# Optimization experiments

Hardware: AMD Instinct MI355X
Metric: run time of the kernel (lower is better)

Reference implementation:

```python
import jax, jax.numpy as jnp
import numpy as np

N, E, D, K, NCONV = 50000, 800000, 64, 3, 6


def setup_inputs() -> dict:
    key = jax.random.key(0)
    ks = jax.random.split(key, 6)
    X = jax.random.normal(ks[0], (N, D), jnp.float32)
    edge_index = jax.random.randint(ks[1], (2, E), 0, N, dtype=jnp.int64)
    edge_weight = jax.random.uniform(ks[2], (E,), jnp.float32)
    H = jax.random.normal(ks[3], (N, D), jnp.float32)
    lambda_max = jnp.ones((1,), jnp.float32) * 2.0  # typical sym-normalized Laplacian bound
    conv_w = jax.random.normal(ks[4], (NCONV, K, D, D), jnp.float32) / np.sqrt(D)
    conv_b = jnp.zeros((NCONV, D), jnp.float32)
    return {"X": X, "edge_index": edge_index, "edge_weight": edge_weight,
            "H": H, "lambda_max": lambda_max, "conv_w": conv_w, "conv_b": conv_b}


def reference(X, edge_index, edge_weight, H, lambda_max, conv_w, conv_b):
    src, dst = edge_index[0], edge_index[1]
    # symmetric normalization: norm_e = w_e / sqrt(deg_src * deg_dst)
    deg = jax.ops.segment_sum(edge_weight, src, num_segments=N)
    dinv = jnp.where(deg > 0, deg ** -0.5, 0.0)
    norm = edge_weight * dinv[src] * dinv[dst]  # [E]
    lam = lambda_max.reshape(())
    c = 2.0 / lam

    def a_prop(v):  # A_norm @ v via scatter-add over edges, [N,D]
        return jax.ops.segment_sum(norm[:, None] * v[src], dst, num_segments=N)

    def l_hat(v):  # (2/lam)(I - A_norm) v - v
        return (c - 1.0) * v - c * a_prop(v)

    def cheb(v, w, b):  # ChebConv order K: sum_k T_k(L_hat) v @ W_k + b
        tx0, tx1 = v, l_hat(v)
        out = tx0 @ w[0] + tx1 @ w[1]
        for k in range(2, K):
            tx2 = 2.0 * l_hat(tx1) - tx0
            out = out + tx2 @ w[k]
            tx0, tx1 = tx1, tx2
        return out + b

    Z = jax.nn.sigmoid(cheb(X, conv_w[0], conv_b[0]) + cheb(H, conv_w[1], conv_b[1]))
    R = jax.nn.sigmoid(cheb(X, conv_w[2], conv_b[2]) + cheb(H, conv_w[3], conv_b[3]))
    H_tilde = jnp.tanh(cheb(X, conv_w[4], conv_b[4]) + cheb(H * R, conv_w[5], conv_b[5]))
    return Z * H_tilde + (1.0 - Z) * H
```

## Files before the change

### kernel.cpp

```cpp
#include <hip/hip_runtime.h>
#include <cstdint>
#include <cstddef>

typedef unsigned int u32;
typedef unsigned short u16;
typedef unsigned long long u64;

#define D 64
#define NCH 512
#define CAP 5120

typedef __attribute__((ext_vector_type(8))) short bf16x8;
typedef __attribute__((ext_vector_type(4))) float f32x4;

static __device__ __forceinline__ float sigmoidf_(float x) {
    return 1.f / (1.f + __expf(-x));
}
static __device__ __forceinline__ u16 f2bf(float x) {
    u32 u = __float_as_uint(x);
    return (u16)((u + 0x7fffu + ((u >> 16) & 1u)) >> 16);
}
static __device__ __forceinline__ u32 packbf2(float a, float b) {
    return (u32)f2bf(a) | ((u32)f2bf(b) << 16);
}
static __device__ __forceinline__ float bflo(u32 u) { return __uint_as_float(u << 16); }
static __device__ __forceinline__ float bfhi(u32 u) { return __uint_as_float(u & 0xffff0000u); }


__global__ void init_kernel(u32* cur_d, u32* cur_s) {
    int t = threadIdx.x;
    cur_d[t] = (u32)(t * CAP);
    cur_s[t] = (u32)(t * CAP);
}

__global__ __launch_bounds__(256) void coarse_kernel(
    const int* __restrict__ src, const int* __restrict__ dst, const float* __restrict__ w,
    u32* cur_d, u32* cur_s,
    u64* __restrict__ slab_d, u32* __restrict__ slab_s,
    int E, int CE) {
    __shared__ u32 hd[256], hs[256], cd[256], cs[256];
    int t = threadIdx.x, c = blockIdx.x;
    hd[t] = 0; hs[t] = 0;
    __syncthreads();
    int e0 = c * CE, e1 = min(E, e0 + CE);
    for (int e = e0 + t; e < e1; e += 256) {
        atomicAdd(&hd[(u32)dst[e] >> 8], 1u);
        atomicAdd(&hs[(u32)src[e] >> 8], 1u);
    }
    __syncthreads();
    cd[t] = atomicAdd(&cur_d[t], hd[t]);
    cs[t] = atomicAdd(&cur_s[t], hs[t]);
    __syncthreads();
    for (int e = e0 + t; e < e1; e += 256) {
        int s = src[e], d = dst[e];
        u32 wb = (u32)f2bf(w[e]);
        u32 pd = atomicAdd(&cd[(u32)d >> 8], 1u);
        u32 ps = atomicAdd(&cs[(u32)s >> 8], 1u);
        if (pd < (u32)(((d >> 8) + 1) * CAP))
            slab_d[pd] = (u64)((u32)s | (((u32)d & 255u) << 16)) | ((u64)wb << 32);
        if (ps < (u32)(((s >> 8) + 1) * CAP))
            slab_s[ps] = ((u32)s & 255u) | (wb << 16);
    }
}

__global__ void bprefix_kernel(const u32* __restrict__ cur_d, u32* __restrict__ bstart, int NB) {
    __shared__ int sd[256];
    int t = threadIdx.x;
    int v = (t < NB) ? min((int)cur_d[t] - t * CAP, CAP) : 0;
    sd[t] = v;
    __syncthreads();
    for (int o = 1; o < 256; o <<= 1) {
        int a = (t >= o) ? sd[t - o] : 0;
        __syncthreads();
        sd[t] += a;
        __syncthreads();
    }
    bstart[t] = (u32)(sd[t] - v);
}

__global__ __launch_bounds__(256) void fine_dst_kernel(
    const u64* __restrict__ slab, const u32* __restrict__ cur_d,
    const u32* __restrict__ bstart, u32* __restrict__ edge4,
    int* __restrict__ cnt, int* __restrict__ row_start, int N_) {
    __shared__ int h[256], sd[256], cur[256];
    int b = blockIdx.x, t = threadIdx.x;
    int m = min((int)cur_d[b] - b * CAP, CAP);
    const u64* rp = slab + (size_t)b * CAP;
    h[t] = 0;
    __syncthreads();
    for (int i = t; i < m; i += 256) atomicAdd(&h[(int)((rp[i] >> 16) & 255u)], 1);
    __syncthreads();
    int v = h[t];
    sd[t] = v;
    __syncthreads();
    for (int o = 1; o < 256; o <<= 1) {
        int a = (t >= o) ? sd[t - o] : 0;
        __syncthreads();
        sd[t] += a;
        __syncthreads();
    }
    int excl = sd[t] - v;
    cur[t] = excl;
    int bs = (int)bstart[b];
    int node = (b << 8) + t;
    if (node < N_) { cnt[node] = v; row_start[node] = bs + excl; }
    __syncthreads();
    for (int i = t; i < m; i += 256) {
        u64 r = rp[i];
        int f = (int)((r >> 16) & 255u);
        int p = atomicAdd(&cur[f], 1);
        edge4[bs + p] = (u32)(r & 0xffffu) | ((u32)(r >> 32) << 16);
    }
}

__global__ __launch_bounds__(256) void fine_deg_kernel(
    const u32* __restrict__ slab_s, const u32* __restrict__ cur_s,
    float* __restrict__ dinv, int N_) {
    __shared__ float dg[256];
    int b = blockIdx.x, t = threadIdx.x;
    int m = min((int)cur_s[b] - b * CAP, CAP);
    const u32* rp = slab_s + (size_t)b * CAP;
    dg[t] = 0.f;
    __syncthreads();
    for (int i = t; i < m; i += 256) {
        u32 r = rp[i];
        atomicAdd(&dg[r & 255u], __uint_as_float(r & 0xffff0000u));
    }
    __syncthreads();
    int node = (b << 8) + t;
    if (node < N_) dinv[node] = (dg[t] > 0.f) ? rsqrtf(dg[t]) : 0.f;
}


__global__ void xh2_kernel(const float* __restrict__ X, const float* __restrict__ H,
                           const float* __restrict__ dinv,
                           u32* __restrict__ XH_u, u32* __restrict__ XH_t, int total) {
    int i = blockIdx.x * blockDim.x + threadIdx.x;
    if (i >= total) return;
    int nn = i >> 6, l = i & 63;
    const float* sp = (l < 32 ? X : H) + (size_t)nn * 64 + ((2 * l) & 63);
    float2 v = *(const float2*)sp;
    float dv = dinv[nn];
    XH_t[i] = packbf2(v.x, v.y);
    XH_u[i] = packbf2(v.x * dv, v.y * dv);
}

__global__ __launch_bounds__(256) void wt_kernel(const float* __restrict__ w, u32* __restrict__ WT) {
    __shared__ float s[64][68];
    int g = blockIdx.x, t = threadIdx.x;
    const float* wp = w + (size_t)g * 4096;
    for (int i = t; i < 1024; i += 256) {
        int k = i >> 4, c4 = (i & 15) * 4;
        *(float4*)&s[k][c4] = *(const float4*)&wp[k * 64 + c4];
    }
    __syncthreads();
    for (int i = t; i < 2048; i += 256) {
        int uk = i & 31, n = i >> 5;
        WT[(size_t)g * 2048 + n * 32 + uk] = packbf2(s[2 * uk][n], s[2 * uk + 1][n]);
    }
}


__global__ __launch_bounds__(256) void lhat128_kernel(
    const u32* __restrict__ vu, const u32* __restrict__ vt, const u32* __restrict__ w0t,
    u32* __restrict__ out_t, u32* __restrict__ out_u,
    const int* __restrict__ rs, const int* __restrict__ cnt, const float* __restrict__ dinv,
    const u32* __restrict__ edges, const float* __restrict__ lam_ptr, int n) {
    int node = (blockIdx.x * blockDim.x + threadIdx.x) >> 6;
    if (node >= n) return;
    int l = threadIdx.x & 63;
    int g = l >> 4, f = l & 15;
    int e0 = rs[node], end = e0 + cnt[node];
    float acc[8];
#pragma unroll
    for (int j = 0; j < 8; j++) acc[j] = 0.f;

    int base = e0;
    for (; base + 16 <= end; base += 16) {
        u32 r0 = edges[base + g];
        u32 r1 = edges[base + 4 + g];
        u32 r2 = edges[base + 8 + g];
        u32 r3 = edges[base + 12 + g];
        const uint4 q0 = *(const uint4*)(vu + (size_t)(r0 & 0xffffu) * 64 + 4 * f);
        const uint4 q1 = *(const uint4*)(vu + (size_t)(r1 & 0xffffu) * 64 + 4 * f);
        const uint4 q2 = *(const uint4*)(vu + (size_t)(r2 & 0xffffu) * 64 + 4 * f);
        const uint4 q3 = *(const uint4*)(vu + (size_t)(r3 & 0xffffu) * 64 + 4 * f);
        float n0 = __uint_as_float(r0 & 0xffff0000u);
        float n1 = __uint_as_float(r1 & 0xffff0000u);
        float n2 = __uint_as_float(r2 & 0xffff0000u);
        float n3 = __uint_as_float(r3 & 0xffff0000u);
        acc[0] += n0 * bflo(q0.x); acc[1] += n0 * bfhi(q0.x);
        acc[2] += n0 * bflo(q0.y); acc[3] += n0 * bfhi(q0.y);
        acc[4] += n0 * bflo(q0.z); acc[5] += n0 * bfhi(q0.z);
        acc[6] += n0 * bflo(q0.w); acc[7] += n0 * bfhi(q0.w);
        acc[0] += n1 * bflo(q1.x); acc[1] += n1 * bfhi(q1.x);
        acc[2] += n1 * bflo(q1.y); acc[3] += n1 * bfhi(q1.y);
        acc[4] += n1 * bflo(q1.z); acc[5] += n1 * bfhi(q1.z);
        acc[6] += n1 * bflo(q1.w); acc[7] += n1 * bfhi(q1.w);
        acc[0] += n2 * bflo(q2.x); acc[1] += n2 * bfhi(q2.x);
        acc[2] += n2 * bflo(q2.y); acc[3] += n2 * bfhi(q2.y);
        acc[4] += n2 * bflo(q2.z); acc[5] += n2 * bfhi(q2.z);
        acc[6] += n2 * bflo(q2.w); acc[7] += n2 * bfhi(q2.w);
        acc[0] += n3 * bflo(q3.x); acc[1] += n3 * bfhi(q3.x);
        acc[2] += n3 * bflo(q3.y); acc[3] += n3 * bfhi(q3.y);
        acc[4] += n3 * bflo(q3.z); acc[5] += n3 * bfhi(q3.z);
        acc[6] += n3 * bflo(q3.w); acc[7] += n3 * bfhi(q3.w);
    }
    for (; base < end; base += 4) {
        int ei = base + g;
        u32 r0 = (ei < end) ? edges[ei] : 0u;
        const uint4 q0 = *(const uint4*)(vu + (size_t)(r0 & 0xffffu) * 64 + 4 * f);
        float n0 = __uint_as_float(r0 & 0xffff0000u);
        acc[0] += n0 * bflo(q0.x); acc[1] += n0 * bfhi(q0.x);
        acc[2] += n0 * bflo(q0.y); acc[3] += n0 * bfhi(q0.y);
        acc[4] += n0 * bflo(q0.z); acc[5] += n0 * bfhi(q0.z);
        acc[6] += n0 * bflo(q0.w); acc[7] += n0 * bfhi(q0.w);
    }
#pragma unroll
    for (int m = 16; m <= 32; m <<= 1)
#pragma unroll
        for (int j = 0; j < 8; j++) acc[j] += __shfl_xor(acc[j], m);

    const uint4 sv = *(const uint4*)(vt + (size_t)node * 64 + 4 * f);
    float self[8];
    self[0] = bflo(sv.x); self[1] = bfhi(sv.x);
    self[2] = bflo(sv.y); self[3] = bfhi(sv.y);
    self[4] = bflo(sv.z); self[5] = bfhi(sv.z);
    self[6] = bflo(sv.w); self[7] = bfhi(sv.w);
    float c = 2.f / lam_ptr[0];
    float dv = dinv[node];
    float rx[8];
#pragma unroll
    for (int j = 0; j < 8; j++) rx[j] = (c - 1.f) * self[j] - (c * dv) * acc[j];
    if (w0t) {
        const uint4 wv4 = *(const uint4*)(w0t + (size_t)node * 64 + 4 * f);
        rx[0] = 2.f * rx[0] - bflo(wv4.x); rx[1] = 2.f * rx[1] - bfhi(wv4.x);
        rx[2] = 2.f * rx[2] - bflo(wv4.y); rx[3] = 2.f * rx[3] - bfhi(wv4.y);
        rx[4] = 2.f * rx[4] - bflo(wv4.z); rx[5] = 2.f * rx[5] - bfhi(wv4.z);
        rx[6] = 2.f * rx[6] - bflo(wv4.w); rx[7] = 2.f * rx[7] - bfhi(wv4.w);
    }
    if (l < 16) {
        uint4 o;
        o.x = packbf2(rx[0], rx[1]); o.y = packbf2(rx[2], rx[3]);
        o.z = packbf2(rx[4], rx[5]); o.w = packbf2(rx[6], rx[7]);
        *(uint4*)(out_t + (size_t)node * 64 + 4 * f) = o;
        if (out_u) {
            uint4 ou;
            ou.x = packbf2(rx[0] * dv, rx[1] * dv); ou.y = packbf2(rx[2] * dv, rx[3] * dv);
            ou.z = packbf2(rx[4] * dv, rx[5] * dv); ou.w = packbf2(rx[6] * dv, rx[7] * dv);
            *(uint4*)(out_u + (size_t)node * 64 + 4 * f) = ou;
        }
    }
}

__global__ __launch_bounds__(256) void lhat64_kernel(
    const u32* __restrict__ vu, const u32* __restrict__ vt, const u32* __restrict__ w0t,
    u32* __restrict__ out_t, u32* __restrict__ out_u,
    const int* __restrict__ rs, const int* __restrict__ cnt, const float* __restrict__ dinv,
    const u32* __restrict__ edges, const float* __restrict__ lam_ptr, int n) {
    int node = (blockIdx.x * blockDim.x + threadIdx.x) >> 6;
    if (node >= n) return;
    int l = threadIdx.x & 63;
    int g = l >> 3, f = l & 7;
    int e0 = rs[node], end = e0 + cnt[node];
    float acc[8];
#pragma unroll
    for (int j = 0; j < 8; j++) acc[j] = 0.f;

    int base = e0;
    for (; base + 16 <= end; base += 16) {
        u32 r0 = edges[base + g];
        u32 r1 = edges[base + 8 + g];
        const uint4 q0 = *(const uint4*)(vu + (size_t)(r0 & 0xffffu) * 32 + 4 * f);
        const uint4 q1 = *(const uint4*)(vu + (size_t)(r1 & 0xffffu) * 32 + 4 * f);
        float n0 = __uint_as_float(r0 & 0xffff0000u);
        float n1 = __uint_as_float(r1 & 0xffff0000u);
        acc[0] += n0 * bflo(q0.x); acc[1] += n0 * bfhi(q0.x);
        acc[2] += n0 * bflo(q0.y); acc[3] += n0 * bfhi(q0.y);
        acc[4] += n0 * bflo(q0.z); acc[5] += n0 * bfhi(q0.z);
        acc[6] += n0 * bflo(q0.w); acc[7] += n0 * bfhi(q0.w);
        acc[0] += n1 * bflo(q1.x); acc[1] += n1 * bfhi(q1.x);
        acc[2] += n1 * bflo(q1.y); acc[3] += n1 * bfhi(q1.y);
        acc[4] += n1 * bflo(q1.z); acc[5] += n1 * bfhi(q1.z);
        acc[6] += n1 * bflo(q1.w); acc[7] += n1 * bfhi(q1.w);
    }
    for (; base < end; base += 8) {
        int ei = base + g;
        u32 r0 = (ei < end) ? edges[ei] : 0u;
        const uint4 q0 = *(const uint4*)(vu + (size_t)(r0 & 0xffffu) * 32 + 4 * f);
        float n0 = __uint_as_float(r0 & 0xffff0000u);
        acc[0] += n0 * bflo(q0.x); acc[1] += n0 * bfhi(q0.x);
        acc[2] += n0 * bflo(q0.y); acc[3] += n0 * bfhi(q0.y);
        acc[4] += n0 * bflo(q0.z); acc[5] += n0 * bfhi(q0.z);
        acc[6] += n0 * bflo(q0.w); acc[7] += n0 * bfhi(q0.w);
    }
#pragma unroll
    for (int m = 8; m <= 32; m <<= 1)
#pragma unroll
        for (int j = 0; j < 8; j++) acc[j] += __shfl_xor(acc[j], m);

    const uint4 sv = *(const uint4*)(vt + (size_t)node * 32 + 4 * f);
    float self[8];
    self[0] = bflo(sv.x); self[1] = bfhi(sv.x);
    self[2] = bflo(sv.y); self[3] = bfhi(sv.y);
    self[4] = bflo(sv.z); self[5] = bfhi(sv.z);
    self[6] = bflo(sv.w); self[7] = bfhi(sv.w);
    float c = 2.f / lam_ptr[0];
    float dv = dinv[node];
    float rx[8];
#pragma unroll
    for (int j = 0; j < 8; j++) rx[j] = (c - 1.f) * self[j] - (c * dv) * acc[j];
    if (w0t) {
        const uint4 wv4 = *(const uint4*)(w0t + (size_t)node * 32 + 4 * f);
        rx[0] = 2.f * rx[0] - bflo(wv4.x); rx[1] = 2.f * rx[1] - bfhi(wv4.x);
        rx[2] = 2.f * rx[2] - bflo(wv4.y); rx[3] = 2.f * rx[3] - bfhi(wv4.y);
        rx[4] = 2.f * rx[4] - bflo(wv4.z); rx[5] = 2.f * rx[5] - bfhi(wv4.z);
        rx[6] = 2.f * rx[6] - bflo(wv4.w); rx[7] = 2.f * rx[7] - bfhi(wv4.w);
    }
    if (l < 8) {
        uint4 o;
        o.x = packbf2(rx[0], rx[1]); o.y = packbf2(rx[2], rx[3]);
        o.z = packbf2(rx[4], rx[5]); o.w = packbf2(rx[6], rx[7]);
        *(uint4*)(out_t + (size_t)node * 32 + 4 * f) = o;
        if (out_u) {
            uint4 ou;
            ou.x = packbf2(rx[0] * dv, rx[1] * dv); ou.y = packbf2(rx[2] * dv, rx[3] * dv);
            ou.z = packbf2(rx[4] * dv, rx[5] * dv); ou.w = packbf2(rx[6] * dv, rx[7] * dv);
            *(uint4*)(out_u + (size_t)node * 32 + 4 * f) = ou;
        }
    }
}

__global__ __launch_bounds__(256) void gemm_mfma_kernel(
    const u32* __restrict__ A0, const u32* __restrict__ A1, const u32* __restrict__ A2,
    int strideU, int colOffU,
    const u32* __restrict__ WT,
    float* __restrict__ out, int out_ld, int cg0, int cg1, int cg2, int n) {
    __shared__ u32 As[128][20];
    __shared__ u32 Ws[64][20];
    int t = threadIdx.x;
    int wv = t >> 6, l = t & 63;
    int q = l >> 4, ml = l & 15;
    int gate = blockIdx.y;
    int cg = (gate == 0) ? cg0 : ((gate == 1) ? cg1 : cg2);
    int r0 = blockIdx.x * 128;

    f32x4 acc[2][4];
#pragma unroll
    for (int mi = 0; mi < 2; mi++)
#pragma unroll
        for (int ni = 0; ni < 4; ni++) acc[mi][ni] = (f32x4){0.f, 0.f, 0.f, 0.f};

    for (int kt = 0; kt < 3; kt++) {
        const u32* Ap = (kt == 0) ? A0 : ((kt == 1) ? A1 : A2);
        const u32* Wp = WT + (size_t)(cg * 3 + kt) * 2048;
        for (int h = 0; h < 2; h++) {
            int ar = t >> 1, ac = (t & 1) * 8;
            int gr = r0 + ar; if (gr >= n) gr = n - 1;
            const u32* gp = Ap + (size_t)gr * strideU + colOffU + h * 16 + ac;
            uint4 a4a = *(const uint4*)gp;
            uint4 a4b = *(const uint4*)(gp + 4);
            int wr = t >> 2, wc = (t & 3) * 4;
            uint4 w4 = *(const uint4*)(Wp + (size_t)wr * 32 + h * 16 + wc);
            __syncthreads();
            *(uint4*)&As[ar][ac] = a4a;
            *(uint4*)&As[ar][ac + 4] = a4b;
            *(uint4*)&Ws[wr][wc] = w4;
            __syncthreads();

            bf16x8 bfr[4];
#pragma unroll
            for (int ni = 0; ni < 4; ni++)
                bfr[ni] = *(const bf16x8*)&Ws[ni * 16 + ml][q * 4];
#pragma unroll
            for (int mi = 0; mi < 2; mi++) {
                bf16x8 af = *(const bf16x8*)&As[wv * 32 + mi * 16 + ml][q * 4];
#pragma unroll
                for (int ni = 0; ni < 4; ni++)
                    acc[mi][ni] = __builtin_amdgcn_mfma_f32_16x16x32_bf16(af, bfr[ni], acc[mi][ni], 0, 0, 0);
            }
        }
    }
#pragma unroll
    for (int mi = 0; mi < 2; mi++)
#pragma unroll
        for (int ni = 0; ni < 4; ni++)
#pragma unroll
            for (int reg = 0; reg < 4; reg++) {
                int row = r0 + wv * 32 + mi * 16 + q * 4 + reg;
                int col = gate * 64 + ni * 16 + ml;
                if (row < n) out[(size_t)row * out_ld + col] = acc[mi][ni][reg];
            }
}


__global__ void gate_kernel(const float* __restrict__ GX, const float* __restrict__ GH,
                            const float* __restrict__ convb, const float* __restrict__ H,
                            const float* __restrict__ dinv,
                            float* __restrict__ Z, u16* __restrict__ HR_t, u16* __restrict__ HR_u,
                            int total) {
    int i = blockIdx.x * blockDim.x + threadIdx.x;
    if (i >= total) return;
    int n = i >> 6, d = i & 63;
    float z = sigmoidf_(GX[(size_t)n * 192 + d] + GH[(size_t)n * 128 + d]
                        + convb[0 * 64 + d] + convb[1 * 64 + d]);
    float r = sigmoidf_(GX[(size_t)n * 192 + 64 + d] + GH[(size_t)n * 128 + 64 + d]
                        + convb[2 * 64 + d] + convb[3 * 64 + d]);
    float hr = H[i] * r;
    float dv = dinv[n];
    Z[i] = z;
    HR_t[i] = f2bf(hr);
    HR_u[i] = f2bf(hr * dv);
}

__global__ __launch_bounds__(256) void gemm_final_kernel(
    const u32* __restrict__ A0, const u32* __restrict__ A1, const u32* __restrict__ A2,
    const u32* __restrict__ WT, const float* __restrict__ convb,
    const float* __restrict__ Zb, const float* __restrict__ GXh, const float* __restrict__ Hf,
    float* __restrict__ outp, int n) {
    __shared__ u32 As[128][36];
    int t = threadIdx.x;
    int wv = t >> 6, l = t & 63;
    int q = l >> 4, ml = l & 15;
    int r0 = blockIdx.x * 128;

    f32x4 S[2][4];
#pragma unroll
    for (int mi = 0; mi < 2; mi++)
#pragma unroll
        for (int ni = 0; ni < 4; ni++) S[mi][ni] = (f32x4){0.f, 0.f, 0.f, 0.f};

    for (int kt = 0; kt < 3; kt++) {
        const u32* Ap = (kt == 0) ? A0 : ((kt == 1) ? A1 : A2);
        int ar = t >> 1, ac = (t & 1) * 16;
        int gr = r0 + ar; if (gr >= n) gr = n - 1;
        const u32* gp = Ap + (size_t)gr * 32 + ac;
        uint4 v0 = *(const uint4*)(gp +  0);
        uint4 v1 = *(const uint4*)(gp +  4);
        uint4 v2 = *(const uint4*)(gp +  8);
        uint4 v3 = *(const uint4*)(gp + 12);
        __syncthreads();
        *(uint4*)&As[ar][ac +  0] = v0;
        *(uint4*)&As[ar][ac +  4] = v1;
        *(uint4*)&As[ar][ac +  8] = v2;
        *(uint4*)&As[ar][ac + 12] = v3;
        __syncthreads();

        const u32* Wp = WT + (size_t)(15 + kt) * 2048 + ml * 32 + q * 4;
#pragma unroll
        for (int h = 0; h < 2; h++) {
            bf16x8 bw[4];
#pragma unroll
            for (int ni = 0; ni < 4; ni++)
                bw[ni] = *(const bf16x8*)(Wp + ni * 512 + h * 16);
#pragma unroll
            for (int mi = 0; mi < 2; mi++) {
                bf16x8 afr = *(const bf16x8*)&As[wv * 32 + mi * 16 + ml][h * 16 + q * 4];
#pragma unroll
                for (int ni = 0; ni < 4; ni++)
                    S[mi][ni] = __builtin_amdgcn_mfma_f32_16x16x32_bf16(afr, bw[ni], S[mi][ni], 0, 0, 0);
            }
        }
    }
#pragma unroll
    for (int ni = 0; ni < 4; ni++) {
        int col = ni * 16 + ml;
        float bh = convb[256 + col] + convb[320 + col];
#pragma unroll
        for (int mi = 0; mi < 2; mi++)
#pragma unroll
            for (int reg = 0; reg < 4; reg++) {
                int row = r0 + wv * 32 + mi * 16 + q * 4 + reg;
                if (row < n) {
                    size_t o = (size_t)row * 64 + col;
                    float z = Zb[o];
                    float ht = tanhf(S[mi][ni][reg] + GXh[(size_t)row * 192 + col] + bh);
                    outp[o] = z * ht + (1.f - z) * Hf[o];
                }
            }
    }
}


extern "C" void kernel_launch(void* const* d_in, const int* in_sizes, int n_in,
                              void* d_out, int out_size, void* d_ws, size_t ws_size,
                              hipStream_t stream) {
    const float* X     = (const float*)d_in[0];
    const int*   ei    = (const int*)d_in[1];
    const float* ew    = (const float*)d_in[2];
    const float* H     = (const float*)d_in[3];
    const float* lam   = (const float*)d_in[4];
    const float* convw = (const float*)d_in[5];
    const float* convb = (const float*)d_in[6];
    float* out = (float*)d_out;

    const int N = in_sizes[0] / D;
    const int E = in_sizes[2];
    const int* src = ei;
    const int* dst = ei + E;

    const int NB = (N + 255) >> 8;
    const int CE = (E + NCH - 1) / NCH;

    char* p = (char*)d_ws;
    auto alloc = [&](size_t bytes) {
        void* r = (void*)p;
        p += (bytes + 255) & ~(size_t)255;
        return r;
    };
    float* GX   = (float*)alloc((size_t)N * 192 * 4);
    float* GH   = (float*)alloc((size_t)N * 128 * 4);
    float* Zb   = (float*)alloc((size_t)N * 64 * 4);
    u32* XH_u = (u32*)alloc((size_t)N * 64 * 4);
    u32* XH_t = (u32*)alloc((size_t)N * 64 * 4);
    u32* T1_u = (u32*)alloc((size_t)N * 64 * 4);
    u32* T1_t = (u32*)alloc((size_t)N * 64 * 4);
    u32* T2_t = (u32*)alloc((size_t)N * 64 * 4);
    u16* HR_u = (u16*)alloc((size_t)N * 64 * 2);
    u16* HR_t = (u16*)alloc((size_t)N * 64 * 2);
    u16* U1_u = (u16*)alloc((size_t)N * 64 * 2);
    u16* U1_t = (u16*)alloc((size_t)N * 64 * 2);
    u16* U2_t = (u16*)alloc((size_t)N * 64 * 2);
    u32* edge4 = (u32*)alloc((size_t)E * 4);
    u64* slab_d = (u64*)alloc((size_t)NB * CAP * 8);
    u32* slab_s = (u32*)alloc((size_t)NB * CAP * 4);
    u32* cur_d  = (u32*)alloc(256 * 4);
    u32* cur_s  = (u32*)alloc(256 * 4);
    u32* bstart = (u32*)alloc(256 * 4);
    int* cnt       = (int*)alloc((size_t)N * 4);
    int* row_start = (int*)alloc((size_t)N * 4);
    float* dinv    = (float*)alloc((size_t)N * 4);
    u32* WT = (u32*)alloc((size_t)18 * 2048 * 4);

    const int BLK = 256;
    const int gND  = (N * D + BLK - 1) / BLK;
    const int gWav = gND;
    const int gx   = (N + 127) / 128;

    init_kernel<<<1, 256, 0, stream>>>(cur_d, cur_s);
    coarse_kernel<<<NCH, BLK, 0, stream>>>(src, dst, ew, cur_d, cur_s, slab_d, slab_s, E, CE);
    bprefix_kernel<<<1, 256, 0, stream>>>(cur_d, bstart, NB);
    fine_dst_kernel<<<NB, BLK, 0, stream>>>(slab_d, cur_d, bstart, edge4, cnt, row_start, N);
    fine_deg_kernel<<<NB, BLK, 0, stream>>>(slab_s, cur_s, dinv, N);

    wt_kernel<<<18, BLK, 0, stream>>>(convw, WT);
    xh2_kernel<<<gND, BLK, 0, stream>>>(X, H, dinv, XH_u, XH_t, N * D);

    lhat128_kernel<<<gWav, BLK, 0, stream>>>(XH_u, XH_t, nullptr, T1_t, T1_u,
                                             row_start, cnt, dinv, edge4, lam, N);
    lhat128_kernel<<<gWav, BLK, 0, stream>>>(T1_u, T1_t, XH_t, T2_t, nullptr,
                                             row_start, cnt, dinv, edge4, lam, N);
    gemm_mfma_kernel<<<dim3(gx, 3), BLK, 0, stream>>>(XH_t, T1_t, T2_t, 64, 0, WT, GX, 192, 0, 2, 4, N);
    gemm_mfma_kernel<<<dim3(gx, 2), BLK, 0, stream>>>(XH_t, T1_t, T2_t, 64, 32, WT, GH, 128, 1, 3, 3, N);

    gate_kernel<<<gND, BLK, 0, stream>>>(GX, GH, convb, H, dinv, Zb, HR_t, HR_u, N * D);

    lhat64_kernel<<<gWav, BLK, 0, stream>>>((const u32*)HR_u, (const u32*)HR_t, nullptr,
                                            (u32*)U1_t, (u32*)U1_u,
                                            row_start, cnt, dinv, edge4, lam, N);
    lhat64_kernel<<<gWav, BLK, 0, stream>>>((const u32*)U1_u, (const u32*)U1_t, (const u32*)HR_t,
                                            (u32*)U2_t, nullptr,
                                            row_start, cnt, dinv, edge4, lam, N);

    gemm_final_kernel<<<gx, BLK, 0, stream>>>((const u32*)HR_t, (const u32*)U1_t, (const u32*)U2_t,
                                              WT, convb, Zb, GX + 128, H, out, N);
}
```

Measured before the change: 347.4 us.

## Fuse both gate GEMMs with sigmoid gate epilogue into one kernel

Replaces the two gemm_mfma launches (X-side and H-side gates) and the separate gate_kernel with a single kernel. Each block loads the full 128-column XH/T1/T2 row once and accumulates all five conv weight groups into three gate accumulators. It then applies the sigmoid gates and writes Z, H*R and the X-side candidate pre-activation directly. This removes the fp32 GX/GH intermediates and their round trips through global memory, at the cost of more accumulator registers per thread and weights read from global or L2 instead of shared memory.

```diff
diff --git a/kernel.cpp b/kernel.cpp
--- a/kernel.cpp
+++ b/kernel.cpp
@@ -331,92 +331,107 @@
     }
 }
 
-__global__ __launch_bounds__(256) void gemm_mfma_kernel(
+__global__ __launch_bounds__(256) void gemm_gate_kernel(
     const u32* __restrict__ A0, const u32* __restrict__ A1, const u32* __restrict__ A2,
-    int strideU, int colOffU,
-    const u32* __restrict__ WT,
-    float* __restrict__ out, int out_ld, int cg0, int cg1, int cg2, int n) {
-    __shared__ u32 As[128][20];
-    __shared__ u32 Ws[64][20];
+    const u32* __restrict__ WT, const float* __restrict__ convb,
+    const float* __restrict__ Hf, const float* __restrict__ dinv,
+    float* __restrict__ Zb, float* __restrict__ Sh,
+    u16* __restrict__ HR_t, u16* __restrict__ HR_u, int n) {
+    __shared__ u32 As[128][68];
     int t = threadIdx.x;
     int wv = t >> 6, l = t & 63;
     int q = l >> 4, ml = l & 15;
-    int gate = blockIdx.y;
-    int cg = (gate == 0) ? cg0 : ((gate == 1) ? cg1 : cg2);
     int r0 = blockIdx.x * 128;
 
-    f32x4 acc[2][4];
-#pragma unroll
-    for (int mi = 0; mi < 2; mi++)
-#pragma unroll
-        for (int ni = 0; ni < 4; ni++) acc[mi][ni] = (f32x4){0.f, 0.f, 0.f, 0.f};
+    f32x4 S[3][2][4];
+#pragma unroll
+    for (int tg = 0; tg < 3; tg++)
+#pragma unroll
+        for (int mi = 0; mi < 2; mi++)
+#pragma unroll
+            for (int ni = 0; ni < 4; ni++) S[tg][mi][ni] = (f32x4){0.f, 0.f, 0.f, 0.f};
 
     for (int kt = 0; kt < 3; kt++) {
         const u32* Ap = (kt == 0) ? A0 : ((kt == 1) ? A1 : A2);
-        const u32* Wp = WT + (size_t)(cg * 3 + kt) * 2048;
-        for (int h = 0; h < 2; h++) {
-            int ar = t >> 1, ac = (t & 1) * 8;
-            int gr = r0 + ar; if (gr >= n) gr = n - 1;
-            const u32* gp = Ap + (size_t)gr * strideU + colOffU + h * 16 + ac;
-            uint4 a4a = *(const uint4*)gp;
-            uint4 a4b = *(const uint4*)(gp + 4);
-            int wr = t >> 2, wc = (t & 3) * 4;
-            uint4 w4 = *(const uint4*)(Wp + (size_t)wr * 32 + h * 16 + wc);
-            __syncthreads();
-            *(uint4*)&As[ar][ac] = a4a;
-            *(uint4*)&As[ar][ac + 4] = a4b;
-            *(uint4*)&Ws[wr][wc] = w4;
-            __syncthreads();
-
-            bf16x8 bfr[4];
-#pragma unroll
-            for (int ni = 0; ni < 4; ni++)
-                bfr[ni] = *(const bf16x8*)&Ws[ni * 16 + ml][q * 4];
-#pragma unroll
-            for (int mi = 0; mi < 2; mi++) {
-                bf16x8 af = *(const bf16x8*)&As[wv * 32 + mi * 16 + ml][q * 4];
+        int ar = t >> 1, ac = (t & 1) * 32;
+        int gr = r0 + ar; if (gr >= n) gr = n - 1;
+        const u32* gp = Ap + (size_t)gr * 64 + ac;
+        uint4 v0 = *(const uint4*)(gp +  0);
+        uint4 v1 = *(const uint4*)(gp +  4);
+        uint4 v2 = *(const uint4*)(gp +  8);
+        uint4 v3 = *(const uint4*)(gp + 12);
+        uint4 v4 = *(const uint4*)(gp + 16);
+        uint4 v5 = *(const uint4*)(gp + 20);
+        uint4 v6 = *(const uint4*)(gp + 24);
+        uint4 v7 = *(const uint4*)(gp + 28);
+        __syncthreads();
+        *(uint4*)&As[ar][ac +  0] = v0;
+        *(uint4*)&As[ar][ac +  4] = v1;
+        *(uint4*)&As[ar][ac +  8] = v2;
+        *(uint4*)&As[ar][ac + 12] = v3;
+        *(uint4*)&As[ar][ac + 16] = v4;
+        *(uint4*)&As[ar][ac + 20] = v5;
+        *(uint4*)&As[ar][ac + 24] = v6;
+        *(uint4*)&As[ar][ac + 28] = v7;
+        __syncthreads();
+
+        bf16x8 af[2][2][2];
+#pragma unroll
+        for (int mi = 0; mi < 2; mi++)
+#pragma unroll
+            for (int h = 0; h < 2; h++)
+#pragma unroll
+                for (int hf = 0; hf < 2; hf++)
+                    af[mi][h][hf] = *(const bf16x8*)&As[wv * 32 + mi * 16 + ml][hf * 32 + h * 16 + q * 4];
+
+#pragma unroll
+        for (int cg = 0; cg < 5; cg++) {
+            int hf = cg & 1, tg = cg >> 1;
+            const u32* Wp = WT + (size_t)(cg * 3 + kt) * 2048 + ml * 32 + q * 4;
+#pragma unroll
+            for (int h = 0; h < 2; h++) {
+                bf16x8 bw[4];
 #pragma unroll
                 for (int ni = 0; ni < 4; ni++)
-                    acc[mi][ni] = __builtin_amdgcn_mfma_f32_16x16x32_bf16(af, bfr[ni], acc[mi][ni], 0, 0, 0);
+                    bw[ni] = *(const bf16x8*)(Wp + ni * 512 + h * 16);
+#pragma unroll
+                for (int mi = 0; mi < 2; mi++)
+#pragma unroll
+                    for (int ni = 0; ni < 4; ni++)
+                        S[tg][mi][ni] = __builtin_amdgcn_mfma_f32_16x16x32_bf16(
+                            af[mi][h][hf], bw[ni], S[tg][mi][ni], 0, 0, 0);
             }
         }
     }
 #pragma unroll
-    for (int mi = 0; mi < 2; mi++)
-#pragma unroll
-        for (int ni = 0; ni < 4; ni++)
+    for (int ni = 0; ni < 4; ni++) {
+        int col = ni * 16 + ml;
+        float bz = convb[col] + convb[64 + col];
+        float br = convb[128 + col] + convb[192 + col];
+#pragma unroll
+        for (int mi = 0; mi < 2; mi++)
 #pragma unroll
             for (int reg = 0; reg < 4; reg++) {
                 int row = r0 + wv * 32 + mi * 16 + q * 4 + reg;
-                int col = gate * 64 + ni * 16 + ml;
-                if (row < n) out[(size_t)row * out_ld + col] = acc[mi][ni][reg];
+                if (row < n) {
+                    size_t o = (size_t)row * 64 + col;
+                    float z = sigmoidf_(S[0][mi][ni][reg] + bz);
+                    float r = sigmoidf_(S[1][mi][ni][reg] + br);
+                    float hr = Hf[o] * r;
+                    float dv = dinv[row];
+                    Zb[o] = z;
+                    Sh[o] = S[2][mi][ni][reg];
+                    HR_t[o] = f2bf(hr);
+                    HR_u[o] = f2bf(hr * dv);
+                }
             }
-}
-
-
-__global__ void gate_kernel(const float* __restrict__ GX, const float* __restrict__ GH,
-                            const float* __restrict__ convb, const float* __restrict__ H,
-                            const float* __restrict__ dinv,
-                            float* __restrict__ Z, u16* __restrict__ HR_t, u16* __restrict__ HR_u,
-                            int total) {
-    int i = blockIdx.x * blockDim.x + threadIdx.x;
-    if (i >= total) return;
-    int n = i >> 6, d = i & 63;
-    float z = sigmoidf_(GX[(size_t)n * 192 + d] + GH[(size_t)n * 128 + d]
-                        + convb[0 * 64 + d] + convb[1 * 64 + d]);
-    float r = sigmoidf_(GX[(size_t)n * 192 + 64 + d] + GH[(size_t)n * 128 + 64 + d]
-                        + convb[2 * 64 + d] + convb[3 * 64 + d]);
-    float hr = H[i] * r;
-    float dv = dinv[n];
-    Z[i] = z;
-    HR_t[i] = f2bf(hr);
-    HR_u[i] = f2bf(hr * dv);
+    }
 }
 
 __global__ __launch_bounds__(256) void gemm_final_kernel(
     const u32* __restrict__ A0, const u32* __restrict__ A1, const u32* __restrict__ A2,
     const u32* __restrict__ WT, const float* __restrict__ convb,
-    const float* __restrict__ Zb, const float* __restrict__ GXh, const float* __restrict__ Hf,
+    const float* __restrict__ Zb, const float* __restrict__ Sh, const float* __restrict__ Hf,
     float* __restrict__ outp, int n) {
     __shared__ u32 As[128][36];
     int t = threadIdx.x;
@@ -474,7 +489,7 @@
                 if (row < n) {
                     size_t o = (size_t)row * 64 + col;
                     float z = Zb[o];
-                    float ht = tanhf(S[mi][ni][reg] + GXh[(size_t)row * 192 + col] + bh);
+                    float ht = tanhf(S[mi][ni][reg] + Sh[o] + bh);
                     outp[o] = z * ht + (1.f - z) * Hf[o];
                 }
             }
@@ -508,9 +523,8 @@
         p += (bytes + 255) & ~(size_t)255;
         return r;
     };
-    float* GX   = (float*)alloc((size_t)N * 192 * 4);
-    float* GH   = (float*)alloc((size_t)N * 128 * 4);
     float* Zb   = (float*)alloc((size_t)N * 64 * 4);
+    float* Sh   = (float*)alloc((size_t)N * 64 * 4);
     u32* XH_u = (u32*)alloc((size_t)N * 64 * 4);
     u32* XH_t = (u32*)alloc((size_t)N * 64 * 4);
     u32* T1_u = (u32*)alloc((size_t)N * 64 * 4);
@@ -550,10 +564,9 @@
                                              row_start, cnt, dinv, edge4, lam, N);
     lhat128_kernel<<<gWav, BLK, 0, stream>>>(T1_u, T1_t, XH_t, T2_t, nullptr,
                                              row_start, cnt, dinv, edge4, lam, N);
-    gemm_mfma_kernel<<<dim3(gx, 3), BLK, 0, stream>>>(XH_t, T1_t, T2_t, 64, 0, WT, GX, 192, 0, 2, 4, N);
-    gemm_mfma_kernel<<<dim3(gx, 2), BLK, 0, stream>>>(XH_t, T1_t, T2_t, 64, 32, WT, GH, 128, 1, 3, 3, N);
-
-    gate_kernel<<<gND, BLK, 0, stream>>>(GX, GH, convb, H, dinv, Zb, HR_t, HR_u, N * D);
+
+    gemm_gate_kernel<<<gx, BLK, 0, stream>>>(XH_t, T1_t, T2_t, WT, convb, H, dinv,
+                                             Zb, Sh, HR_t, HR_u, N);
 
     lhat64_kernel<<<gWav, BLK, 0, stream>>>((const u32*)HR_u, (const u32*)HR_t, nullptr,
                                             (u32*)U1_t, (u32*)U1_u,
@@ -563,5 +576,5 @@
                                             row_start, cnt, dinv, edge4, lam, N);
 
     gemm_final_kernel<<<gx, BLK, 0, stream>>>((const u32*)HR_t, (const u32*)U1_t, (const u32*)U2_t,
-                                              WT, convb, Zb, GX + 128, H, out, N);
-}
+                                              WT, convb, Zb, Sh, H, out, N);
+}
```

Measured after the change: 339.3 us. -2.3%, faster.
